# Kernel optimization log

Hardware: AMD Instinct MI355X
Metric: run time of the kernel (lower is better)

Reference implementation:

```python
import jax, jax.numpy as jnp
import numpy as np

N, D_IN, D_OUT, NHEAD = 4096, 512, 128, 4


def setup_inputs() -> dict:
    key = jax.random.key(0)
    k1, k2, k3, k4, k5 = jax.random.split(key, 5)
    adj = jax.random.randint(k1, (N, N), 0, 2).astype(jnp.float32)  # dense binary adjacency
    x = jax.random.normal(k2, (N, D_IN), dtype=jnp.float32)
    W = jax.random.normal(k3, (D_IN, D_OUT), dtype=jnp.float32) * (1.0 / np.sqrt(D_IN))
    attn_l_w = jax.random.normal(k4, (NHEAD, D_OUT), dtype=jnp.float32) * (1.0 / np.sqrt(D_OUT))
    attn_r_w = jax.random.normal(k5, (NHEAD, D_OUT), dtype=jnp.float32) * (1.0 / np.sqrt(D_OUT))
    b = jnp.zeros((D_OUT,), dtype=jnp.float32)
    return {"adj": adj, "x": x, "W": W, "attn_l_w": attn_l_w, "attn_r_w": attn_r_w, "b": b}


def reference(adj, x, W, attn_l_w, attn_r_w, b):
    # h = x @ W : [N, D_OUT]
    h = x @ W
    el = h @ attn_l_w.T  # [N, H]  (nn.Linear(output_dim, nhead, bias=False))
    er = h @ attn_r_w.T  # [N, H]
    # Dense equivalent of nonzero-gather + index_put_ scatter into [N, N, H]:
    # attn[i, j, :] = exp(leaky_relu(el[i] + er[j])) where adj[i, j] != 0, else 0.
    e = el[:, None, :] + er[None, :, :]                      # [N, N, H]
    a = jnp.where(adj[:, :, None] != 0,
                  jnp.exp(jax.nn.leaky_relu(e, negative_slope=0.2)),
                  jnp.zeros((), dtype=e.dtype))              # [N, N, H]
    a = jnp.transpose(a, (0, 2, 1))                          # [N, H, N]
    # F.normalize(p=1, dim=-1): divide by max(L1 row sum, 1e-12); a >= 0 so L1 = sum.
    a = a / jnp.maximum(jnp.sum(a, axis=-1, keepdims=True), 1e-12)
    out = jnp.einsum('nhm,md->nhd', a, h) + b                # [N, H, D_OUT]
    return out.reshape(out.shape[0], -1)                     # flatten heads -> [N, H*D_OUT]
```

## Files before the change

### kernel.cpp

```cpp
#include <hip/hip_runtime.h>

#define NN 4096
#define DIN 512
#define DOUT 128
#define NH 4
#define LOG2E 1.44269504088896340736f

typedef __bf16 bf16x8 __attribute__((ext_vector_type(8)));
typedef float f32x4 __attribute__((ext_vector_type(4)));
typedef float f32x16 __attribute__((ext_vector_type(16)));
typedef unsigned short u16;
typedef unsigned int u32;
typedef unsigned long long u64;
typedef u16 u16x8 __attribute__((ext_vector_type(8)));
typedef u16 u16x4 __attribute__((ext_vector_type(4)));

static __device__ __forceinline__ u16 f2bf(float f) {
  __bf16 h = (__bf16)f;
  return __builtin_bit_cast(u16, h);
}

static __device__ __forceinline__ void gl_lds16(const void* g, void* l) {
  __builtin_amdgcn_global_load_lds(
      (const __attribute__((address_space(1))) unsigned int*)g,
      (__attribute__((address_space(3))) unsigned int*)l, 16, 0, 0);
}

__global__ __launch_bounds__(256) void pack_prep(const float* __restrict__ adj,
                                                 u64* __restrict__ adjW,
                                                 const float* __restrict__ W,
                                                 u16* __restrict__ wthi,
                                                 u16* __restrict__ wtlo) {
  const int b = blockIdx.x;
  const int t = threadIdx.x;
  if (b < 2048) {
    const int wv = t >> 6, lane = t & 63;
    const int gw = b * 4 + wv;
    const int r = gw >> 1, hf = gw & 1;
    const float* src = adj + (size_t)r * NN + hf * 2048 + lane;
    u64* dstw = adjW + (size_t)r * 64 + hf * 32;
    #pragma unroll 4
    for (int it = 0; it < 32; ++it) {
      const u64 m = __ballot(src[it * 64] != 0.f);
      if (lane == 0) dstw[it] = m;
    }
  } else {
    const int n = b - 2048;
    for (int k = t; k < 512; k += 256) {
      const float w = W[(size_t)k * 128 + n];
      const __bf16 hi = (__bf16)w;
      wthi[(size_t)n * 512 + k] = __builtin_bit_cast(u16, hi);
      wtlo[(size_t)n * 512 + k] = f2bf(w - (float)hi);
    }
  }
}

__global__ __launch_bounds__(512, 1) void hcompute(
    const float* __restrict__ x, const u16* __restrict__ wthi,
    const u16* __restrict__ wtlo, const float* __restrict__ alw,
    const float* __restrict__ arw, u16x8* __restrict__ hTf,
    float* __restrict__ elP, float* __restrict__ elp,
    float* __restrict__ erQ, float* __restrict__ erq) {
  __shared__ __align__(16) char pool[147456];
  const int t = threadIdx.x;
  const int i0 = blockIdx.x * 16;
  const int lane = t & 63, w = t >> 6;
  const int l15 = lane & 15, lhi = lane >> 4;

  const int xr = t >> 5, xk = (t & 31) * 4;
  const unsigned x_off =
      ((unsigned)(xr * 256 + xk * 2)) ^ ((unsigned)((xr & 7) << 4));

  f32x4 acc = (f32x4){0.f, 0.f, 0.f, 0.f};

  auto stageW = [&](int kc, int buf) {
    #pragma unroll
    for (int q = 0; q < 4; ++q) {
      const int off = q * 8192 + t * 16;
      const int n = off >> 8;
      const int kb = off & 255;
      const int ksrc = (kb ^ ((n & 7) << 4)) >> 1;
      const size_t so = (size_t)n * 512 + kc * 128 + ksrc;
      gl_lds16(wthi + so, pool + 16384 + buf * 32768 + off);
      gl_lds16(wtlo + so, pool + 81920 + buf * 32768 + off);
    }
  };
  auto writeX = [&](const float4& xv, int buf) {
    u16x4 hi, lo;
    const float* xp = (const float*)&xv;
    #pragma unroll
    for (int j = 0; j < 4; ++j) {
      const __bf16 hb = (__bf16)xp[j];
      hi[j] = __builtin_bit_cast(u16, hb);
      lo[j] = f2bf(xp[j] - (float)hb);
    }
    *(u16x4*)(pool + buf * 4096 + x_off) = hi;
    *(u16x4*)(pool + 8192 + buf * 4096 + x_off) = lo;
  };

  stageW(0, 0);
  {
    float4 xv = *(const float4*)(x + (size_t)(i0 + xr) * DIN + xk);
    writeX(xv, 0);
  }
  float4 xnext;
  for (int kc = 0; kc < 4; ++kc) {
    const int cur = kc & 1;
    __syncthreads();
    const bool more = (kc < 3);
    if (more) {
      stageW(kc + 1, cur ^ 1);
      xnext = *(const float4*)(x + (size_t)(i0 + xr) * DIN + (kc + 1) * 128 + xk);
    }
    #pragma unroll
    for (int ks = 0; ks < 4; ++ks) {
      const unsigned kbyte = (unsigned)(ks * 64 + lhi * 16);
      const unsigned xoff =
          (unsigned)(l15 * 256) + (kbyte ^ (unsigned)((l15 & 7) << 4));
      const bf16x8 ah = *(const bf16x8*)(pool + cur * 4096 + xoff);
      const bf16x8 al = *(const bf16x8*)(pool + 8192 + cur * 4096 + xoff);
      const int n = w * 16 + l15;
      const unsigned wb =
          (unsigned)(n * 256) + (kbyte ^ (unsigned)((n & 7) << 4));
      const bf16x8 bh = *(const bf16x8*)(pool + 16384 + cur * 32768 + wb);
      const bf16x8 bl = *(const bf16x8*)(pool + 81920 + cur * 32768 + wb);
      acc = __builtin_amdgcn_mfma_f32_16x16x32_bf16(ah, bh, acc, 0, 0, 0);
      acc = __builtin_amdgcn_mfma_f32_16x16x32_bf16(al, bh, acc, 0, 0, 0);
      acc = __builtin_amdgcn_mfma_f32_16x16x32_bf16(ah, bl, acc, 0, 0, 0);
    }
    if (more) writeX(xnext, cur ^ 1);
  }
  __syncthreads();
  float* h_lds = (float*)(pool + 16384);
  #pragma unroll
  for (int reg = 0; reg < 4; ++reg)
    h_lds[(lhi * 4 + reg) * 132 + w * 16 + l15] = acc[reg];
  __syncthreads();
  if (t < 256) {
    const int d = t >> 1, c8 = t & 1;
    const int j0 = c8 * 8;
    u16x8 hv;
    #pragma unroll
    for (int q = 0; q < 8; ++q) hv[q] = f2bf(h_lds[(j0 + q) * 132 + d]);
    const int jt = i0 >> 6;
    const int w8 = ((i0 >> 3) & 7) + c8;
    const int kt = w8 >> 1, lb = w8 & 1;
    const int ct = d >> 5;
    const int l = lb * 32 + (d & 31);
    hTf[(size_t)((jt * 16 + ct * 4 + kt) * 64 + l)] = hv;
  }
  if (t < 128) {
    const int r = t >> 3, hh = (t >> 1) & 3, side = t & 1;
    const float* wrow = (side ? arw : alw) + hh * DOUT;
    float s = 0.f;
    for (int d = 0; d < 128; ++d) s += h_lds[r * 132 + d] * wrow[d];
    s *= LOG2E;
    const float e1 = exp2f(s), e2 = exp2f(0.2f * s);
    if (side == 0) {
      elP[(size_t)(i0 + r) * NH + hh] = e1;
      elp[(size_t)(i0 + r) * NH + hh] = e2;
    } else {
      erQ[(size_t)hh * NN + i0 + r] = e1;
      erq[(size_t)hh * NN + i0 + r] = e2;
    }
  }
}

__global__ __launch_bounds__(512, 2) void gat_main(
    const unsigned char* __restrict__ adjB, const u16x8* __restrict__ Bf,
    const float* __restrict__ elP, const float* __restrict__ elp,
    const float* __restrict__ erQ, const float* __restrict__ erq,
    const float* __restrict__ bias, float* __restrict__ outp) {
  __shared__ float red[2][4096];
  __shared__ float S_lds[64];
  const int t = threadIdx.x;
  const int i0 = blockIdx.x * 16;
  const int lane = t & 63;
  const int w = t >> 6;
  const int rt = (w >> 2) & 1;
  const int kkg = w & 3;
  const int l31 = lane & 31;
  const int lh = lane >> 5;
  const int il = l31 & 15;
  const int head = rt * 2 + (l31 >> 4);
  if (t < 64) S_lds[t] = 0.f;
  __syncthreads();
  const float Pv = elP[(size_t)(i0 + il) * NH + head];
  const float pv = elp[(size_t)(i0 + il) * NH + head];
  const unsigned char* adjp = adjB + (size_t)(i0 + il) * 512 + kkg * 2 + lh;
  const float* Qp = erQ + (size_t)head * NN + kkg * 16 + lh * 8;
  const float* qp = erq + (size_t)head * NN + kkg * 16 + lh * 8;
  const int fbase = kkg * 64 + lane;

  f32x16 acc0, acc1, acc2, acc3, accS;
  #pragma unroll
  for (int q = 0; q < 16; ++q) {
    acc0[q] = 0.f; acc1[q] = 0.f; acc2[q] = 0.f; acc3[q] = 0.f; accS[q] = 0.f;
  }
  u16x8 onesu;
  #pragma unroll
  for (int q = 0; q < 8; ++q) onesu[q] = 0x3F80;
  const bf16x8 onesf = __builtin_bit_cast(bf16x8, onesu);

  auto loadP = [&](int jt, float4& Q0, float4& Q1, float4& q0, float4& q1,
                   u32& ab, u16x8& b0, u16x8& b1, u16x8& b2, u16x8& b3) {
    const float* Qj = Qp + jt * 64;
    const float* qj = qp + jt * 64;
    Q0 = *(const float4*)Qj;
    Q1 = *(const float4*)(Qj + 4);
    q0 = *(const float4*)qj;
    q1 = *(const float4*)(qj + 4);
    ab = adjp[jt * 8];
    const u16x8* fb = Bf + jt * 1024 + fbase;
    b0 = fb[0];
    b1 = fb[256];
    b2 = fb[512];
    b3 = fb[768];
  };
  auto computeP = [&](const float4& Q0, const float4& Q1, const float4& q0,
                      const float4& q1, u32 ab, const u16x8& b0,
                      const u16x8& b1, const u16x8& b2, const u16x8& b3) {
    float Qv[8], qv[8];
    *(float4*)Qv = Q0;
    *(float4*)(Qv + 4) = Q1;
    *(float4*)qv = q0;
    *(float4*)(qv + 4) = q1;
    u16x8 pk;
    #pragma unroll
    for (int q = 0; q < 8; ++q) {
      const float v = fmaxf(Pv * Qv[q], pv * qv[q]);
      const int msk = ((int)(ab << (31 - q))) >> 31;
      pk[q] = f2bf(__builtin_bit_cast(float, __builtin_bit_cast(int, v) & msk));
    }
    const bf16x8 af = __builtin_bit_cast(bf16x8, pk);
    __builtin_amdgcn_s_setprio(1);
    accS = __builtin_amdgcn_mfma_f32_32x32x16_bf16(af, onesf, accS, 0, 0, 0);
    acc0 = __builtin_amdgcn_mfma_f32_32x32x16_bf16(
        af, __builtin_bit_cast(bf16x8, b0), acc0, 0, 0, 0);
    acc1 = __builtin_amdgcn_mfma_f32_32x32x16_bf16(
        af, __builtin_bit_cast(bf16x8, b1), acc1, 0, 0, 0);
    acc2 = __builtin_amdgcn_mfma_f32_32x32x16_bf16(
        af, __builtin_bit_cast(bf16x8, b2), acc2, 0, 0, 0);
    acc3 = __builtin_amdgcn_mfma_f32_32x32x16_bf16(
        af, __builtin_bit_cast(bf16x8, b3), acc3, 0, 0, 0);
    __builtin_amdgcn_s_setprio(0);
  };

  float4 Q0A, Q1A, q0A, q1A, Q0B, Q1B, q0B, q1B;
  u32 abA, abB;
  u16x8 b0A, b1A, b2A, b3A, b0B, b1B, b2B, b3B;
  loadP(0, Q0A, Q1A, q0A, q1A, abA, b0A, b1A, b2A, b3A);
  for (int pp = 0; pp < 32; ++pp) {
    loadP(2 * pp + 1, Q0B, Q1B, q0B, q1B, abB, b0B, b1B, b2B, b3B);
    computeP(Q0A, Q1A, q0A, q1A, abA, b0A, b1A, b2A, b3A);
    if (pp < 31)
      loadP(2 * pp + 2, Q0A, Q1A, q0A, q1A, abA, b0A, b1A, b2A, b3A);
    computeP(Q0B, Q1B, q0B, q1B, abB, b0B, b1B, b2B, b3B);
  }

  if (l31 == 0) {
    #pragma unroll
    for (int reg = 0; reg < 16; ++reg) {
      const int crow = (reg & 3) + 8 * (reg >> 2) + 4 * lh;
      atomicAdd(&S_lds[rt * 32 + crow], accS[reg]);
    }
  }
  auto wr1 = [&](f32x16& a, int ct) {
    float* dst = red[rt] + ct * 1024 + lane * 4;
    #pragma unroll
    for (int q4 = 0; q4 < 4; ++q4)
      *(f32x4*)(dst + q4 * 256) =
          (f32x4){a[q4 * 4], a[q4 * 4 + 1], a[q4 * 4 + 2], a[q4 * 4 + 3]};
  };
  auto ad1 = [&](f32x16& a, int ct) {
    const float* s = red[rt] + ct * 1024 + lane * 4;
    #pragma unroll
    for (int q4 = 0; q4 < 4; ++q4) {
      const f32x4 v = *(const f32x4*)(s + q4 * 256);
      a[q4 * 4] += v[0];
      a[q4 * 4 + 1] += v[1];
      a[q4 * 4 + 2] += v[2];
      a[q4 * 4 + 3] += v[3];
    }
  };
  auto writeAcc = [&]() { wr1(acc0, 0); wr1(acc1, 1); wr1(acc2, 2); wr1(acc3, 3); };
  auto addAcc = [&]() { ad1(acc0, 0); ad1(acc1, 1); ad1(acc2, 2); ad1(acc3, 3); };

  __syncthreads();
  if (kkg == 1) writeAcc();
  __syncthreads();
  if (kkg == 0) addAcc();
  __syncthreads();
  if (kkg == 3) writeAcc();
  __syncthreads();
  if (kkg == 2) addAcc();
  __syncthreads();
  if (kkg == 2) writeAcc();
  __syncthreads();
  auto st1 = [&](f32x16& a, int ct) {
    const int col = ct * 32 + l31;
    const float bb = bias[col];
    #pragma unroll
    for (int reg = 0; reg < 16; ++reg) {
      const int crow = (reg & 3) + 8 * (reg >> 2) + 4 * lh;
      const int mrow = rt * 32 + crow;
      const float inv = 1.f / fmaxf(S_lds[mrow], 1e-12f);
      outp[(size_t)(i0 + (mrow & 15)) * (NH * DOUT) + (mrow >> 4) * DOUT + col] =
          a[reg] * inv + bb;
    }
  };
  if (kkg == 0) {
    addAcc();
    st1(acc0, 0);
    st1(acc1, 1);
    st1(acc2, 2);
    st1(acc3, 3);
  }
}

extern "C" void kernel_launch(void* const* d_in, const int* in_sizes, int n_in,
                              void* d_out, int out_size, void* d_ws, size_t ws_size,
                              hipStream_t stream) {
  const float* adj = (const float*)d_in[0];
  const float* x = (const float*)d_in[1];
  const float* W = (const float*)d_in[2];
  const float* alw = (const float*)d_in[3];
  const float* arw = (const float*)d_in[4];
  const float* bias = (const float*)d_in[5];
  float* out = (float*)d_out;
  char* ws = (char*)d_ws;
  u16x8* hTf = (u16x8*)ws;
  float* elP = (float*)(ws + 0x100000);
  float* elp = (float*)(ws + 0x110000);
  float* erQ = (float*)(ws + 0x120000);
  float* erq = (float*)(ws + 0x130000);
  unsigned char* adjB = (unsigned char*)(ws + 0x140000);
  u16* wthi = (u16*)(ws + 0x340000);
  u16* wtlo = (u16*)(ws + 0x360000);

  pack_prep<<<2176, 256, 0, stream>>>(adj, (u64*)adjB, W, wthi, wtlo);
  hcompute<<<256, 512, 0, stream>>>(x, wthi, wtlo, alw, arw, hTf, elP, elp, erQ, erq);
  gat_main<<<256, 512, 0, stream>>>(adjB, (const u16x8*)hTf, elP, elp, erQ, erq,
                                    bias, out);
}
```

Measured before the change: 180.1 us.

## Split neighbor loop across twice the waves and reduce partials with LDS atomics

Doubles the block size to 1024 threads and gives each wave pair half of the neighbor (j) tiles, so each wave does half the MFMA work and more waves hide latency. The row-sum MFMA against a ones vector is replaced by a scalar running sum on the VALU, combined with a shuffle and LDS atomics. The staged multi-barrier tree reduction of accumulators becomes LDS atomicAdd into a zeroed buffer, followed by a cooperative all-thread epilogue for normalization and bias. The cost is many LDS float atomics and tighter register limits from the new launch bounds, which could cause spills.

```diff
diff --git a/kernel.cpp b/kernel.cpp
--- a/kernel.cpp
+++ b/kernel.cpp
@@ -166,44 +166,53 @@
   }
 }
 
-__global__ __launch_bounds__(512, 2) void gat_main(
+__global__ __launch_bounds__(1024, 4) void gat_main(
     const unsigned char* __restrict__ adjB, const u16x8* __restrict__ Bf,
     const float* __restrict__ elP, const float* __restrict__ elp,
     const float* __restrict__ erQ, const float* __restrict__ erq,
     const float* __restrict__ bias, float* __restrict__ outp) {
-  __shared__ float red[2][4096];
+  __shared__ float red[8192];
   __shared__ float S_lds[64];
   const int t = threadIdx.x;
   const int i0 = blockIdx.x * 16;
   const int lane = t & 63;
   const int w = t >> 6;
-  const int rt = (w >> 2) & 1;
-  const int kkg = w & 3;
+  const int rt = w >> 3;
+  const int kkg = (w >> 1) & 3;
+  const int jh = w & 1;
   const int l31 = lane & 31;
   const int lh = lane >> 5;
   const int il = l31 & 15;
   const int head = rt * 2 + (l31 >> 4);
+
+  *(f32x4*)(red + t * 8) = (f32x4){0.f, 0.f, 0.f, 0.f};
+  *(f32x4*)(red + t * 8 + 4) = (f32x4){0.f, 0.f, 0.f, 0.f};
   if (t < 64) S_lds[t] = 0.f;
   __syncthreads();
-  const float Pv = elP[(size_t)(i0 + il) * NH + head];
-  const float pv = elp[(size_t)(i0 + il) * NH + head];
-  const unsigned char* adjp = adjB + (size_t)(i0 + il) * 512 + kkg * 2 + lh;
-  const float* Qp = erQ + (size_t)head * NN + kkg * 16 + lh * 8;
-  const float* qp = erq + (size_t)head * NN + kkg * 16 + lh * 8;
-  const int fbase = kkg * 64 + lane;
-
-  f32x16 acc0, acc1, acc2, acc3, accS;
+
+  const float Pv = elP[(i0 + il) * NH + head];
+  const float pv = elp[(i0 + il) * NH + head];
+  const unsigned char* adjp = adjB + (i0 + il) * 512 + kkg * 2 + lh;
+  const float* Qp = erQ + head * NN + kkg * 16 + lh * 8;
+  const float* qp = erq + head * NN + kkg * 16 + lh * 8;
+  const int fB = kkg * 64 + lane;
+
+  f32x16 acc0, acc1, acc2, acc3;
   #pragma unroll
-  for (int q = 0; q < 16; ++q) {
-    acc0[q] = 0.f; acc1[q] = 0.f; acc2[q] = 0.f; acc3[q] = 0.f; accS[q] = 0.f;
-  }
-  u16x8 onesu;
-  #pragma unroll
-  for (int q = 0; q < 8; ++q) onesu[q] = 0x3F80;
-  const bf16x8 onesf = __builtin_bit_cast(bf16x8, onesu);
-
-  auto loadP = [&](int jt, float4& Q0, float4& Q1, float4& q0, float4& q1,
-                   u32& ab, u16x8& b0, u16x8& b1, u16x8& b2, u16x8& b3) {
+  for (int q = 0; q < 16; ++q) { acc0[q] = 0.f; acc1[q] = 0.f; acc2[q] = 0.f; acc3[q] = 0.f; }
+  float Sp = 0.f;
+  const int jbase = jh * 32;
+
+  u16x8 a0, a1, a2, a3, c0, c1, c2, c3;
+  auto loadB = [&](int jt, u16x8& b0, u16x8& b1, u16x8& b2, u16x8& b3) {
+    const u16x8* fb = Bf + jt * 1024 + fB;
+    b0 = fb[0];
+    b1 = fb[256];
+    b2 = fb[512];
+    b3 = fb[768];
+  };
+  auto loadQ = [&](int jt, float4& Q0, float4& Q1, float4& q0, float4& q1,
+                   u32& ab) {
     const float* Qj = Qp + jt * 64;
     const float* qj = qp + jt * 64;
     Q0 = *(const float4*)Qj;
@@ -211,15 +220,10 @@
     q0 = *(const float4*)qj;
     q1 = *(const float4*)(qj + 4);
     ab = adjp[jt * 8];
-    const u16x8* fb = Bf + jt * 1024 + fbase;
-    b0 = fb[0];
-    b1 = fb[256];
-    b2 = fb[512];
-    b3 = fb[768];
-  };
-  auto computeP = [&](const float4& Q0, const float4& Q1, const float4& q0,
-                      const float4& q1, u32 ab, const u16x8& b0,
-                      const u16x8& b1, const u16x8& b2, const u16x8& b3) {
+  };
+  auto compute = [&](const float4& Q0, const float4& Q1, const float4& q0,
+                     const float4& q1, u32 ab, const u16x8& b0, const u16x8& b1,
+                     const u16x8& b2, const u16x8& b3) {
     float Qv[8], qv[8];
     *(float4*)Qv = Q0;
     *(float4*)(Qv + 4) = Q1;
@@ -230,11 +234,13 @@
     for (int q = 0; q < 8; ++q) {
       const float v = fmaxf(Pv * Qv[q], pv * qv[q]);
       const int msk = ((int)(ab << (31 - q))) >> 31;
-      pk[q] = f2bf(__builtin_bit_cast(float, __builtin_bit_cast(int, v) & msk));
+      const float avf =
+          __builtin_bit_cast(float, __builtin_bit_cast(int, v) & msk);
+      Sp += avf;
+      pk[q] = f2bf(avf);
     }
     const bf16x8 af = __builtin_bit_cast(bf16x8, pk);
     __builtin_amdgcn_s_setprio(1);
-    accS = __builtin_amdgcn_mfma_f32_32x32x16_bf16(af, onesf, accS, 0, 0, 0);
     acc0 = __builtin_amdgcn_mfma_f32_32x32x16_bf16(
         af, __builtin_bit_cast(bf16x8, b0), acc0, 0, 0, 0);
     acc1 = __builtin_amdgcn_mfma_f32_32x32x16_bf16(
@@ -246,75 +252,45 @@
     __builtin_amdgcn_s_setprio(0);
   };
 
-  float4 Q0A, Q1A, q0A, q1A, Q0B, Q1B, q0B, q1B;
-  u32 abA, abB;
-  u16x8 b0A, b1A, b2A, b3A, b0B, b1B, b2B, b3B;
-  loadP(0, Q0A, Q1A, q0A, q1A, abA, b0A, b1A, b2A, b3A);
-  for (int pp = 0; pp < 32; ++pp) {
-    loadP(2 * pp + 1, Q0B, Q1B, q0B, q1B, abB, b0B, b1B, b2B, b3B);
-    computeP(Q0A, Q1A, q0A, q1A, abA, b0A, b1A, b2A, b3A);
-    if (pp < 31)
-      loadP(2 * pp + 2, Q0A, Q1A, q0A, q1A, abA, b0A, b1A, b2A, b3A);
-    computeP(Q0B, Q1B, q0B, q1B, abB, b0B, b1B, b2B, b3B);
-  }
-
-  if (l31 == 0) {
+  loadB(jbase, a0, a1, a2, a3);
+  float4 Q0, Q1, q0, q1;
+  u32 ab;
+  for (int pp = 0; pp < 16; ++pp) {
+    const int jA = jbase + 2 * pp;
+    loadQ(jA, Q0, Q1, q0, q1, ab);
+    loadB(jA + 1, c0, c1, c2, c3);
+    compute(Q0, Q1, q0, q1, ab, a0, a1, a2, a3);
+    loadQ(jA + 1, Q0, Q1, q0, q1, ab);
+    loadB(jA + 2, a0, a1, a2, a3);
+    compute(Q0, Q1, q0, q1, ab, c0, c1, c2, c3);
+  }
+
+  Sp += __shfl_xor(Sp, 32);
+  if (lane < 32) atomicAdd(&S_lds[rt * 32 + l31], Sp);
+  float* rb = red + rt * 4096;
+  {
     #pragma unroll
     for (int reg = 0; reg < 16; ++reg) {
       const int crow = (reg & 3) + 8 * (reg >> 2) + 4 * lh;
-      atomicAdd(&S_lds[rt * 32 + crow], accS[reg]);
-    }
-  }
-  auto wr1 = [&](f32x16& a, int ct) {
-    float* dst = red[rt] + ct * 1024 + lane * 4;
-    #pragma unroll
-    for (int q4 = 0; q4 < 4; ++q4)
-      *(f32x4*)(dst + q4 * 256) =
-          (f32x4){a[q4 * 4], a[q4 * 4 + 1], a[q4 * 4 + 2], a[q4 * 4 + 3]};
-  };
-  auto ad1 = [&](f32x16& a, int ct) {
-    const float* s = red[rt] + ct * 1024 + lane * 4;
-    #pragma unroll
-    for (int q4 = 0; q4 < 4; ++q4) {
-      const f32x4 v = *(const f32x4*)(s + q4 * 256);
-      a[q4 * 4] += v[0];
-      a[q4 * 4 + 1] += v[1];
-      a[q4 * 4 + 2] += v[2];
-      a[q4 * 4 + 3] += v[3];
-    }
-  };
-  auto writeAcc = [&]() { wr1(acc0, 0); wr1(acc1, 1); wr1(acc2, 2); wr1(acc3, 3); };
-  auto addAcc = [&]() { ad1(acc0, 0); ad1(acc1, 1); ad1(acc2, 2); ad1(acc3, 3); };
-
+      float* rr = rb + crow * 128 + l31;
+      atomicAdd(rr + 0, acc0[reg]);
+      atomicAdd(rr + 32, acc1[reg]);
+      atomicAdd(rr + 64, acc2[reg]);
+      atomicAdd(rr + 96, acc3[reg]);
+    }
+  }
   __syncthreads();
-  if (kkg == 1) writeAcc();
-  __syncthreads();
-  if (kkg == 0) addAcc();
-  __syncthreads();
-  if (kkg == 3) writeAcc();
-  __syncthreads();
-  if (kkg == 2) addAcc();
-  __syncthreads();
-  if (kkg == 2) writeAcc();
-  __syncthreads();
-  auto st1 = [&](f32x16& a, int ct) {
-    const int col = ct * 32 + l31;
-    const float bb = bias[col];
-    #pragma unroll
-    for (int reg = 0; reg < 16; ++reg) {
-      const int crow = (reg & 3) + 8 * (reg >> 2) + 4 * lh;
-      const int mrow = rt * 32 + crow;
-      const float inv = 1.f / fmaxf(S_lds[mrow], 1e-12f);
-      outp[(size_t)(i0 + (mrow & 15)) * (NH * DOUT) + (mrow >> 4) * DOUT + col] =
-          a[reg] * inv + bb;
-    }
-  };
-  if (kkg == 0) {
-    addAcc();
-    st1(acc0, 0);
-    st1(acc1, 1);
-    st1(acc2, 2);
-    st1(acc3, 3);
+  {
+    const int e = t * 8;
+    const int col = e & 127;
+    const int mrow = e >> 7;
+    const float inv = 1.f / fmaxf(S_lds[mrow], 1e-12f);
+    const float* rp = red + mrow * 128 + col;
+    const float* bp = bias + col;
+    float* op = outp + (size_t)(i0 + (mrow & 15)) * (NH * DOUT) +
+                (mrow >> 4) * DOUT + col;
+    #pragma unroll
+    for (int j = 0; j < 8; ++j) op[j] = rp[j] * inv + bp[j];
   }
 }
 
@@ -340,6 +316,6 @@
 
   pack_prep<<<2176, 256, 0, stream>>>(adj, (u64*)adjB, W, wthi, wtlo);
   hcompute<<<256, 512, 0, stream>>>(x, wthi, wtlo, alw, arw, hTf, elP, elp, erQ, erq);
-  gat_main<<<256, 512, 0, stream>>>(adjB, (const u16x8*)hTf, elP, elp, erQ, erq,
-                                    bias, out);
-}
+  gat_main<<<256, 1024, 0, stream>>>(adjB, (const u16x8*)hTf, elP, elp, erQ, erq,
+                                     bias, out);
+}
```

Measured after the change: 274.4 us. 52.4% more time.
